# Optimization experiments

Hardware: AMD Instinct MI355X
Metric: run time of the kernel (lower is better)

The kernel has to match this reference:

```python
import jax, jax.numpy as jnp
import numpy as np

B, N, K, C = 4, 8192, 16, 64
HID, OUT = 128, 128


def setup_inputs() -> dict:
    key = jax.random.key(0)
    ks = jax.random.split(key, 8)
    f = jax.random.normal(ks[0], (B, N, C), dtype=jnp.float32)
    knn_idx = jax.random.randint(ks[1], (B, N, K), 0, N, dtype=jnp.int32)
    W1 = jax.random.normal(ks[2], (3 * C, HID), dtype=jnp.float32) * (1.0 / np.sqrt(3 * C))
    b1 = jnp.zeros((HID,), dtype=jnp.float32)
    W2 = jax.random.normal(ks[3], (HID, HID), dtype=jnp.float32) * (1.0 / np.sqrt(HID))
    b2 = jnp.zeros((HID,), dtype=jnp.float32)
    W3 = jax.random.normal(ks[4], (HID, OUT), dtype=jnp.float32) * 0.05  # init.normal_(std=0.05)
    b3 = jnp.zeros((OUT,), dtype=jnp.float32)  # init.zeros_
    return {"f": f, "knn_idx": knn_idx, "W1": W1, "b1": b1, "W2": W2, "b2": b2, "W3": W3, "b3": b3}


def reference(f, knn_idx, W1, b1, W2, b2, W3, b3):
    # knn_group: gather neighbor features -> [B, N, k, C]
    knn_feat = jax.vmap(lambda fb, ib: fb[ib])(f, knn_idx)
    f_tiled = jnp.broadcast_to(f[:, :, None, :], knn_feat.shape)  # [B,N,k,C]
    x = jnp.concatenate([f_tiled, knn_feat, knn_feat - f_tiled], axis=-1)  # [B,N,k,3C]
    x = jax.nn.relu(jnp.einsum('bnkc,ch->bnkh', x, W1) + b1)
    x = jax.nn.relu(jnp.einsum('bnkh,hg->bnkg', x, W2) + b2)
    x = jnp.max(x, axis=2)  # max-pool over k -> [B,N,HID]
    return jnp.einsum('bnh,ho->bno', x, W3) + b3
```

## Files before the change

### kernel.cpp

```cpp
#include <hip/hip_runtime.h>


#define BB 4
#define NN 8192
#define KK 16
#define CC 64
#define HH 128
#define ITERS 4

typedef _Float16 f16;
typedef __fp16 h16x2 __attribute__((ext_vector_type(2)));
typedef _Float16 f16x8 __attribute__((ext_vector_type(8)));
typedef float f32x4 __attribute__((ext_vector_type(4)));

#define MFMA16(a, b, c) __builtin_amdgcn_mfma_f32_16x16x32_f16(a, b, c, 0, 0, 0)

static __device__ __forceinline__ f16x8 cvt8(f32x4 a0, f32x4 a1) {
  h16x2 c0 = __builtin_amdgcn_cvt_pkrtz(a0[0], a0[1]);
  h16x2 c1 = __builtin_amdgcn_cvt_pkrtz(a0[2], a0[3]);
  h16x2 c2 = __builtin_amdgcn_cvt_pkrtz(a1[0], a1[1]);
  h16x2 c3 = __builtin_amdgcn_cvt_pkrtz(a1[2], a1[3]);
  f16x8 v;
  v[0] = (f16)c0[0]; v[1] = (f16)c0[1]; v[2] = (f16)c1[0]; v[3] = (f16)c1[1];
  v[4] = (f16)c2[0]; v[5] = (f16)c2[1]; v[6] = (f16)c3[0]; v[7] = (f16)c3[1];
  return v;
}

static __device__ __forceinline__ void lds_barrier() {
  asm volatile("s_waitcnt lgkmcnt(0)" ::: "memory");
  __builtin_amdgcn_s_barrier();
  __builtin_amdgcn_sched_barrier(0);
}

__global__ void prep_all(const float* __restrict__ f, const float* __restrict__ W1,
                         const float* __restrict__ W2, const float* __restrict__ W3,
                         f16* __restrict__ ws, f16* __restrict__ fh) {
  if (blockIdx.x < 12) {
    int fid = blockIdx.x * 8 + (threadIdx.x >> 6);
    int l = threadIdx.x & 63;
    int g = l >> 4, r = l & 15;
    f16x8 v;
#pragma unroll
    for (int j = 0; j < 8; ++j) {
      int kl = 16 * (j >> 2) + 4 * g + (j & 3);
      float x;
      if (fid < 16) {
        int ht = fid >> 1, kt = fid & 1, h = ht * 16 + r, k = kt * 32 + kl;
        x = W1[(64 + k) * HH + h] + W1[(128 + k) * HH + h];
      } else if (fid < 48) {
        int t = fid - 16, h2t = t >> 2, kt = t & 3;
        x = W2[(kt * 32 + kl) * HH + h2t * 16 + r];
      } else if (fid < 64) {
        int t = fid - 48, ht = t >> 1, kt = t & 1, h = ht * 16 + r, k = kt * 32 + kl;
        x = W1[k * HH + h] - W1[(128 + k) * HH + h];
      } else {
        int t = fid - 64, ot = t >> 2, kt = t & 3;
        x = W3[(kt * 32 + kl) * HH + ot * 16 + r];
      }
      v[j] = (f16)x;
    }
    *(f16x8*)(ws + (size_t)fid * 512 + l * 8) = v;
  } else {
    int chunk = (blockIdx.x - 12) * 512 + threadIdx.x;
    int row = chunk >> 3;
    int kt = (chunk >> 2) & 1;
    int g = chunk & 3;
    const float* src = f + (size_t)row * CC + kt * 32;
    f32x4 a0 = *(const f32x4*)(src + 4 * g);
    f32x4 a1 = *(const f32x4*)(src + 16 + 4 * g);
    f16x8 v;
#pragma unroll
    for (int j = 0; j < 4; ++j) { v[j] = (f16)a0[j]; v[4 + j] = (f16)a1[j]; }
    *(f16x8*)(fh + (size_t)row * CC + kt * 32 + g * 8) = v;
  }
}

__global__ __launch_bounds__(512, 4) void knn_pers(
    const int* __restrict__ knn, const float* __restrict__ b1,
    const float* __restrict__ b2, const float* __restrict__ b3,
    const f16* __restrict__ ws, const f16* __restrict__ fh,
    float* __restrict__ out) {
  extern __shared__ char smem[];
  f16* wbuf = (f16*)smem;
  float* fabuf = (float*)(wbuf + 48 * 512);
  f16* pooled = (f16*)(fabuf + 16 * 132);

  const int tid = threadIdx.x;
  const int wave = tid >> 6, lane = tid & 63;
  const int g = lane >> 4, r = lane & 15;

  const int wg = (blockIdx.x & 7) * 64 + (blockIdx.x >> 3);
  const int b = wg >> 7;
  const int nbase = (wg & 127) * 64;
  const f16* fhb = fh + (size_t)b * NN * CC;
  const int p0 = wave * 2;

  f16x8 st[6];
#pragma unroll
  for (int i = 0; i < 6; ++i)
    st[i] = *(const f16x8*)(ws + (size_t)(i * 512 + tid) * 8);
#pragma unroll
  for (int i = 0; i < 6; ++i)
    *(f16x8*)(wbuf + (size_t)(i * 512 + tid) * 8) = st[i];

  f16x8 aw[2], w3f[4];
#pragma unroll
  for (int kt = 0; kt < 2; ++kt)
    aw[kt] = *(const f16x8*)(ws + (size_t)(48 + wave * 2 + kt) * 512 + lane * 8);
#pragma unroll
  for (int kt = 0; kt < 4; ++kt)
    w3f[kt] = *(const f16x8*)(ws + (size_t)(64 + wave * 4 + kt) * 512 + lane * 8);

  int nidx[2];
#pragma unroll
  for (int pp = 0; pp < 2; ++pp)
    nidx[pp] = knn[(size_t)(b * NN + nbase + p0 + pp) * KK + r];
  f16x8 bfa[2];
  {
    const f16* fo16 = fhb + (size_t)(nbase + r) * CC;
    bfa[0] = *(const f16x8*)(fo16 + g * 8);
    bfa[1] = *(const f16x8*)(fo16 + 32 + g * 8);
  }
  f16x8 bf[2][2];
#pragma unroll
  for (int pp = 0; pp < 2; ++pp) {
    const f16* fn16 = fhb + (size_t)nidx[pp] * CC;
#pragma unroll
    for (int kt = 0; kt < 2; ++kt)
      bf[pp][kt] = *(const f16x8*)(fn16 + kt * 32 + g * 8);
  }

  for (int it = 0; it < ITERS; ++it) {
    const int n0 = nbase + it * 16;
    const int itn = (it < ITERS - 1) ? it + 1 : it;

    int nidxN[2];
#pragma unroll
    for (int pp = 0; pp < 2; ++pp)
      nidxN[pp] = knn[(size_t)(b * NN + nbase + itn * 16 + p0 + pp) * KK + r];

    {
      f32x4 acc = {0.f, 0.f, 0.f, 0.f};
      acc = MFMA16(aw[0], bfa[0], acc);
      acc = MFMA16(aw[1], bfa[1], acc);
      f32x4 b1v = *(const f32x4*)(b1 + wave * 16 + g * 4);
      f32x4 fa;
#pragma unroll
      for (int i = 0; i < 4; ++i) fa[i] = acc[i] + b1v[i];
      *(f32x4*)(fabuf + r * 132 + wave * 16 + g * 4) = fa;
    }

    lds_barrier();

    f16x8 h1f[2][4];
#pragma unroll
    for (int ht = 0; ht < 8; ++ht) {
      f32x4 acc[2] = {{0.f, 0.f, 0.f, 0.f}, {0.f, 0.f, 0.f, 0.f}};
#pragma unroll
      for (int kt = 0; kt < 2; ++kt) {
        f16x8 wfrag = *(const f16x8*)(wbuf + (size_t)(ht * 2 + kt) * 512 + lane * 8);
        acc[0] = MFMA16(wfrag, bf[0][kt], acc[0]);
        acc[1] = MFMA16(wfrag, bf[1][kt], acc[1]);
      }
      f32x4 fa0 = *(const f32x4*)(fabuf + (p0 + 0) * 132 + ht * 16 + g * 4);
      f32x4 fa1 = *(const f32x4*)(fabuf + (p0 + 1) * 132 + ht * 16 + g * 4);
#pragma unroll
      for (int pp = 0; pp < 2; ++pp) {
        const f32x4& fa = pp ? fa1 : fa0;
        float x0 = acc[pp][0] + fa[0]; x0 = x0 > 0.f ? x0 : 0.f;
        float x1 = acc[pp][1] + fa[1]; x1 = x1 > 0.f ? x1 : 0.f;
        float x2 = acc[pp][2] + fa[2]; x2 = x2 > 0.f ? x2 : 0.f;
        float x3 = acc[pp][3] + fa[3]; x3 = x3 > 0.f ? x3 : 0.f;
        h16x2 lo = __builtin_amdgcn_cvt_pkrtz(x0, x1);
        h16x2 hi = __builtin_amdgcn_cvt_pkrtz(x2, x3);
        h1f[pp][ht >> 1][(ht & 1) * 4 + 0] = (f16)lo[0];
        h1f[pp][ht >> 1][(ht & 1) * 4 + 1] = (f16)lo[1];
        h1f[pp][ht >> 1][(ht & 1) * 4 + 2] = (f16)hi[0];
        h1f[pp][ht >> 1][(ht & 1) * 4 + 3] = (f16)hi[1];
      }
    }

#pragma unroll
    for (int h2t = 0; h2t < 8; ++h2t) {
      f32x4 c0 = {0.f, 0.f, 0.f, 0.f}, c1 = {0.f, 0.f, 0.f, 0.f};
#pragma unroll
      for (int kt = 0; kt < 4; ++kt) {
        f16x8 w2f = *(const f16x8*)(wbuf + (size_t)(16 + h2t * 4 + kt) * 512 + lane * 8);
        c0 = MFMA16(h1f[0][kt], w2f, c0);
        c1 = MFMA16(h1f[1][kt], w2f, c1);
      }
      float b2v = b2[h2t * 16 + r];
#pragma unroll
      for (int pp = 0; pp < 2; ++pp) {
        f32x4 cc = pp ? c1 : c0;
        float m = fmaxf(fmaxf(cc[0], cc[1]), fmaxf(cc[2], cc[3]));
        m = fmaxf(m, __shfl_xor(m, 16, 64));
        m = fmaxf(m, __shfl_xor(m, 32, 64));
        float x = m + b2v;
        f16 pv = (f16)(x > 0.f ? x : 0.f);
        if (g == 0) {
          pooled[(h2t >> 1) * 512 + ((r >> 2) * 16 + p0 + pp) * 8 +
                 (h2t & 1) * 4 + (r & 3)] = pv;
        }
      }
    }

    f16x8 bfaN[2], bfN[2][2];
    {
      const f16* fo16 = fhb + (size_t)(nbase + itn * 16 + r) * CC;
      bfaN[0] = *(const f16x8*)(fo16 + g * 8);
      bfaN[1] = *(const f16x8*)(fo16 + 32 + g * 8);
    }
#pragma unroll
    for (int pp = 0; pp < 2; ++pp) {
      const f16* fn16 = fhb + (size_t)nidxN[pp] * CC;
#pragma unroll
      for (int kt = 0; kt < 2; ++kt)
        bfN[pp][kt] = *(const f16x8*)(fn16 + kt * 32 + g * 8);
    }

    lds_barrier();

    {
      f32x4 a3 = {0.f, 0.f, 0.f, 0.f};
#pragma unroll
      for (int kt = 0; kt < 4; ++kt) {
        f16x8 pf = *(const f16x8*)(pooled + kt * 512 + lane * 8);
        a3 = MFMA16(w3f[kt], pf, a3);
      }
      f32x4 b3v = *(const f32x4*)(b3 + wave * 16 + g * 4);
      f32x4 o;
#pragma unroll
      for (int i = 0; i < 4; ++i) o[i] = a3[i] + b3v[i];
      *(f32x4*)(out + ((size_t)b * NN + n0 + r) * HH + wave * 16 + g * 4) = o;
    }

    bfa[0] = bfaN[0]; bfa[1] = bfaN[1];
#pragma unroll
    for (int pp = 0; pp < 2; ++pp)
#pragma unroll
      for (int kt = 0; kt < 2; ++kt)
        bf[pp][kt] = bfN[pp][kt];
    nidx[0] = nidxN[0]; nidx[1] = nidxN[1];
  }
}

__global__ __launch_bounds__(512, 4) void knn_fb(
    const float* __restrict__ f, const int* __restrict__ knn,
    const float* __restrict__ b1, const float* __restrict__ b2,
    const float* __restrict__ b3, const f16* __restrict__ ws,
    float* __restrict__ out) {
  extern __shared__ char smem[];
  f16* wbuf = (f16*)smem;
  float* fabuf = (float*)(wbuf + 48 * 512);
  f16* pooled = (f16*)(fabuf + 16 * 132);

  const int tid = threadIdx.x;
  const int wave = tid >> 6, lane = tid & 63;
  const int g = lane >> 4, r = lane & 15;
  const int wg = (blockIdx.x & 7) * 256 + (blockIdx.x >> 3);
  const int b = wg >> 9;
  const int n0 = (wg & 511) * 16;
  const float* fb = f + (size_t)b * NN * CC;
  const int p0 = wave * 2;

  int nidx[2];
#pragma unroll
  for (int pp = 0; pp < 2; ++pp)
    nidx[pp] = knn[(size_t)(b * NN + n0 + p0 + pp) * KK + r];

  const float* fo = fb + (size_t)(n0 + r) * CC;
  f32x4 rawF[2][2];
#pragma unroll
  for (int kt = 0; kt < 2; ++kt) {
    rawF[kt][0] = *(const f32x4*)(fo + kt * 32 + 4 * g);
    rawF[kt][1] = *(const f32x4*)(fo + kt * 32 + 4 * g + 16);
  }
  f16x8 aw[2];
#pragma unroll
  for (int kt = 0; kt < 2; ++kt)
    aw[kt] = *(const f16x8*)(ws + (size_t)(48 + wave * 2 + kt) * 512 + lane * 8);

  f16x8 st[6];
#pragma unroll
  for (int i = 0; i < 6; ++i)
    st[i] = *(const f16x8*)(ws + (size_t)(i * 512 + tid) * 8);
#pragma unroll
  for (int i = 0; i < 6; ++i)
    *(f16x8*)(wbuf + (size_t)(i * 512 + tid) * 8) = st[i];

  f32x4 rawN[2][2][2];
#pragma unroll
  for (int pp = 0; pp < 2; ++pp) {
    const float* fn = fb + (size_t)nidx[pp] * CC;
#pragma unroll
    for (int kt = 0; kt < 2; ++kt) {
      rawN[pp][kt][0] = *(const f32x4*)(fn + kt * 32 + 4 * g);
      rawN[pp][kt][1] = *(const f32x4*)(fn + kt * 32 + 4 * g + 16);
    }
  }

  {
    f32x4 acc = {0.f, 0.f, 0.f, 0.f};
#pragma unroll
    for (int kt = 0; kt < 2; ++kt) {
      f16x8 bfa2 = cvt8(rawF[kt][0], rawF[kt][1]);
      acc = MFMA16(aw[kt], bfa2, acc);
    }
    f32x4 b1v = *(const f32x4*)(b1 + wave * 16 + g * 4);
    f32x4 fa;
#pragma unroll
    for (int i = 0; i < 4; ++i) fa[i] = acc[i] + b1v[i];
    *(f32x4*)(fabuf + r * 132 + wave * 16 + g * 4) = fa;
  }

  lds_barrier();

  f16x8 bf[2][2];
#pragma unroll
  for (int pp = 0; pp < 2; ++pp)
#pragma unroll
    for (int kt = 0; kt < 2; ++kt)
      bf[pp][kt] = cvt8(rawN[pp][kt][0], rawN[pp][kt][1]);

  f16x8 h1f[2][4];
#pragma unroll
  for (int ht = 0; ht < 8; ++ht) {
    f32x4 acc[2] = {{0.f, 0.f, 0.f, 0.f}, {0.f, 0.f, 0.f, 0.f}};
#pragma unroll
    for (int kt = 0; kt < 2; ++kt) {
      f16x8 wfrag = *(const f16x8*)(wbuf + (size_t)(ht * 2 + kt) * 512 + lane * 8);
      acc[0] = MFMA16(wfrag, bf[0][kt], acc[0]);
      acc[1] = MFMA16(wfrag, bf[1][kt], acc[1]);
    }
    f32x4 fa0 = *(const f32x4*)(fabuf + (p0 + 0) * 132 + ht * 16 + g * 4);
    f32x4 fa1 = *(const f32x4*)(fabuf + (p0 + 1) * 132 + ht * 16 + g * 4);
#pragma unroll
    for (int pp = 0; pp < 2; ++pp) {
      const f32x4& fa = pp ? fa1 : fa0;
      float x0 = acc[pp][0] + fa[0]; x0 = x0 > 0.f ? x0 : 0.f;
      float x1 = acc[pp][1] + fa[1]; x1 = x1 > 0.f ? x1 : 0.f;
      float x2 = acc[pp][2] + fa[2]; x2 = x2 > 0.f ? x2 : 0.f;
      float x3 = acc[pp][3] + fa[3]; x3 = x3 > 0.f ? x3 : 0.f;
      h16x2 lo = __builtin_amdgcn_cvt_pkrtz(x0, x1);
      h16x2 hi = __builtin_amdgcn_cvt_pkrtz(x2, x3);
      h1f[pp][ht >> 1][(ht & 1) * 4 + 0] = (f16)lo[0];
      h1f[pp][ht >> 1][(ht & 1) * 4 + 1] = (f16)lo[1];
      h1f[pp][ht >> 1][(ht & 1) * 4 + 2] = (f16)hi[0];
      h1f[pp][ht >> 1][(ht & 1) * 4 + 3] = (f16)hi[1];
    }
  }

#pragma unroll
  for (int h2t = 0; h2t < 8; ++h2t) {
    f32x4 c0 = {0.f, 0.f, 0.f, 0.f}, c1 = {0.f, 0.f, 0.f, 0.f};
#pragma unroll
    for (int kt = 0; kt < 4; ++kt) {
      f16x8 w2f = *(const f16x8*)(wbuf + (size_t)(16 + h2t * 4 + kt) * 512 + lane * 8);
      c0 = MFMA16(h1f[0][kt], w2f, c0);
      c1 = MFMA16(h1f[1][kt], w2f, c1);
    }
    float b2v = b2[h2t * 16 + r];
#pragma unroll
    for (int pp = 0; pp < 2; ++pp) {
      f32x4 cc = pp ? c1 : c0;
      float m = fmaxf(fmaxf(cc[0], cc[1]), fmaxf(cc[2], cc[3]));
      m = fmaxf(m, __shfl_xor(m, 16, 64));
      m = fmaxf(m, __shfl_xor(m, 32, 64));
      float x = m + b2v;
      f16 pv = (f16)(x > 0.f ? x : 0.f);
      if (g == 0) {
        pooled[(h2t >> 1) * 512 + ((r >> 2) * 16 + p0 + pp) * 8 +
               (h2t & 1) * 4 + (r & 3)] = pv;
      }
    }
  }

  f16x8 w3f[4];
#pragma unroll
  for (int kt = 0; kt < 4; ++kt)
    w3f[kt] = *(const f16x8*)(ws + (size_t)(64 + wave * 4 + kt) * 512 + lane * 8);

  lds_barrier();

  {
    f32x4 a3 = {0.f, 0.f, 0.f, 0.f};
#pragma unroll
    for (int kt = 0; kt < 4; ++kt) {
      f16x8 pf = *(const f16x8*)(pooled + kt * 512 + lane * 8);
      a3 = MFMA16(w3f[kt], pf, a3);
    }
    f32x4 b3v = *(const f32x4*)(b3 + wave * 16 + g * 4);
    f32x4 o;
#pragma unroll
    for (int i = 0; i < 4; ++i) o[i] = a3[i] + b3v[i];
    *(f32x4*)(out + ((size_t)b * NN + n0 + r) * HH + wave * 16 + g * 4) = o;
  }
}

extern "C" void kernel_launch(void* const* d_in, const int* in_sizes, int n_in,
                              void* d_out, int out_size, void* d_ws, size_t ws_size,
                              hipStream_t stream) {
  const float* f = (const float*)d_in[0];
  const int* knn = (const int*)d_in[1];
  const float* W1 = (const float*)d_in[2];
  const float* b1 = (const float*)d_in[3];
  const float* W2 = (const float*)d_in[4];
  const float* b2 = (const float*)d_in[5];
  const float* W3 = (const float*)d_in[6];
  const float* b3 = (const float*)d_in[7];
  float* outp = (float*)d_out;
  f16* wsp = (f16*)d_ws;
  f16* fh = wsp + 96 * 512;

  const size_t need = 96 * 1024 + (size_t)BB * NN * CC * 2;

  if (ws_size >= need) {
    (void)hipFuncSetAttribute((const void*)knn_pers,
                              hipFuncAttributeMaxDynamicSharedMemorySize, 61696);
    prep_all<<<12 + (BB * NN * 8) / 512, 512, 0, stream>>>(f, W1, W2, W3, wsp, fh);
    knn_pers<<<(BB * NN) / 64, 512, 61696, stream>>>(knn, b1, b2, b3, wsp, fh, outp);
  } else {
    (void)hipFuncSetAttribute((const void*)knn_fb,
                              hipFuncAttributeMaxDynamicSharedMemorySize, 61696);
    prep_all<<<12, 512, 0, stream>>>(f, W1, W2, W3, wsp, fh);
    knn_fb<<<(BB * NN) / 16, 512, 61696, stream>>>(f, knn, b1, b2, b3, wsp, outp);
  }
}
```

Baseline: 44.71 us.

## Double-buffer center-feature and pooled LDS buffers to drop one barrier per iteration

Result: slower. 47.61 us (+6.5%).

```diff
diff --git a/kernel.cpp b/kernel.cpp
--- a/kernel.cpp
+++ b/kernel.cpp
@@ -83,7 +83,7 @@
   extern __shared__ char smem[];
   f16* wbuf = (f16*)smem;
   float* fabuf = (float*)(wbuf + 48 * 512);
-  f16* pooled = (f16*)(fabuf + 16 * 132);
+  f16* pooled = (f16*)(fabuf + 2 * 16 * 132);
 
   const int tid = threadIdx.x;
   const int wave = tid >> 6, lane = tid & 63;
@@ -110,47 +110,57 @@
 #pragma unroll
   for (int kt = 0; kt < 4; ++kt)
     w3f[kt] = *(const f16x8*)(ws + (size_t)(64 + wave * 4 + kt) * 512 + lane * 8);
+  f32x4 b1v = *(const f32x4*)(b1 + wave * 16 + g * 4);
+  f32x4 b3v = *(const f32x4*)(b3 + wave * 16 + g * 4);
+  float b2v[8];
+#pragma unroll
+  for (int h2t = 0; h2t < 8; ++h2t) b2v[h2t] = b2[h2t * 16 + r];
 
   int nidx[2];
 #pragma unroll
   for (int pp = 0; pp < 2; ++pp)
     nidx[pp] = knn[(size_t)(b * NN + nbase + p0 + pp) * KK + r];
-  f16x8 bfa[2];
+  f16x8 bf[2][2];
+#pragma unroll
+  for (int pp = 0; pp < 2; ++pp) {
+    const f16* fn16 = fhb + (size_t)nidx[pp] * CC;
+#pragma unroll
+    for (int kt = 0; kt < 2; ++kt)
+      bf[pp][kt] = *(const f16x8*)(fn16 + kt * 32 + g * 8);
+  }
   {
     const f16* fo16 = fhb + (size_t)(nbase + r) * CC;
-    bfa[0] = *(const f16x8*)(fo16 + g * 8);
-    bfa[1] = *(const f16x8*)(fo16 + 32 + g * 8);
-  }
-  f16x8 bf[2][2];
-#pragma unroll
-  for (int pp = 0; pp < 2; ++pp) {
-    const f16* fn16 = fhb + (size_t)nidx[pp] * CC;
-#pragma unroll
-    for (int kt = 0; kt < 2; ++kt)
-      bf[pp][kt] = *(const f16x8*)(fn16 + kt * 32 + g * 8);
-  }
+    f16x8 a0 = *(const f16x8*)(fo16 + g * 8);
+    f16x8 a1 = *(const f16x8*)(fo16 + 32 + g * 8);
+    f32x4 acc = {0.f, 0.f, 0.f, 0.f};
+    acc = MFMA16(aw[0], a0, acc);
+    acc = MFMA16(aw[1], a1, acc);
+    f32x4 fa;
+#pragma unroll
+    for (int i = 0; i < 4; ++i) fa[i] = acc[i] + b1v[i];
+    *(f32x4*)(fabuf + r * 132 + wave * 16 + g * 4) = fa;
+  }
+
+  lds_barrier();
 
   for (int it = 0; it < ITERS; ++it) {
     const int n0 = nbase + it * 16;
     const int itn = (it < ITERS - 1) ? it + 1 : it;
+    const int cur = it & 1, nxt = (it + 1) & 1;
+    float* fabC = fabuf + cur * 2112;
+    float* fabN = fabuf + nxt * 2112;
+    f16* pooC = pooled + cur * 2048;
 
     int nidxN[2];
 #pragma unroll
     for (int pp = 0; pp < 2; ++pp)
       nidxN[pp] = knn[(size_t)(b * NN + nbase + itn * 16 + p0 + pp) * KK + r];
-
+    f16x8 bfaN0, bfaN1;
     {
-      f32x4 acc = {0.f, 0.f, 0.f, 0.f};
-      acc = MFMA16(aw[0], bfa[0], acc);
-      acc = MFMA16(aw[1], bfa[1], acc);
-      f32x4 b1v = *(const f32x4*)(b1 + wave * 16 + g * 4);
-      f32x4 fa;
-#pragma unroll
-      for (int i = 0; i < 4; ++i) fa[i] = acc[i] + b1v[i];
-      *(f32x4*)(fabuf + r * 132 + wave * 16 + g * 4) = fa;
-    }
-
-    lds_barrier();
+      const f16* fo16 = fhb + (size_t)(nbase + itn * 16 + r) * CC;
+      bfaN0 = *(const f16x8*)(fo16 + g * 8);
+      bfaN1 = *(const f16x8*)(fo16 + 32 + g * 8);
+    }
 
     f16x8 h1f[2][4];
 #pragma unroll
@@ -162,8 +172,8 @@
         acc[0] = MFMA16(wfrag, bf[0][kt], acc[0]);
         acc[1] = MFMA16(wfrag, bf[1][kt], acc[1]);
       }
-      f32x4 fa0 = *(const f32x4*)(fabuf + (p0 + 0) * 132 + ht * 16 + g * 4);
-      f32x4 fa1 = *(const f32x4*)(fabuf + (p0 + 1) * 132 + ht * 16 + g * 4);
+      f32x4 fa0 = *(const f32x4*)(fabC + (p0 + 0) * 132 + ht * 16 + g * 4);
+      f32x4 fa1 = *(const f32x4*)(fabC + (p0 + 1) * 132 + ht * 16 + g * 4);
 #pragma unroll
       for (int pp = 0; pp < 2; ++pp) {
         const f32x4& fa = pp ? fa1 : fa0;
@@ -189,28 +199,32 @@
         c0 = MFMA16(h1f[0][kt], w2f, c0);
         c1 = MFMA16(h1f[1][kt], w2f, c1);
       }
-      float b2v = b2[h2t * 16 + r];
 #pragma unroll
       for (int pp = 0; pp < 2; ++pp) {
         f32x4 cc = pp ? c1 : c0;
         float m = fmaxf(fmaxf(cc[0], cc[1]), fmaxf(cc[2], cc[3]));
         m = fmaxf(m, __shfl_xor(m, 16, 64));
         m = fmaxf(m, __shfl_xor(m, 32, 64));
-        float x = m + b2v;
+        float x = m + b2v[h2t];
         f16 pv = (f16)(x > 0.f ? x : 0.f);
         if (g == 0) {
-          pooled[(h2t >> 1) * 512 + ((r >> 2) * 16 + p0 + pp) * 8 +
-                 (h2t & 1) * 4 + (r & 3)] = pv;
+          pooC[(h2t >> 1) * 512 + ((r >> 2) * 16 + p0 + pp) * 8 +
+               (h2t & 1) * 4 + (r & 3)] = pv;
         }
       }
     }
 
-    f16x8 bfaN[2], bfN[2][2];
     {
-      const f16* fo16 = fhb + (size_t)(nbase + itn * 16 + r) * CC;
-      bfaN[0] = *(const f16x8*)(fo16 + g * 8);
-      bfaN[1] = *(const f16x8*)(fo16 + 32 + g * 8);
-    }
+      f32x4 acc = {0.f, 0.f, 0.f, 0.f};
+      acc = MFMA16(aw[0], bfaN0, acc);
+      acc = MFMA16(aw[1], bfaN1, acc);
+      f32x4 fa;
+#pragma unroll
+      for (int i = 0; i < 4; ++i) fa[i] = acc[i] + b1v[i];
+      *(f32x4*)(fabN + r * 132 + wave * 16 + g * 4) = fa;
+    }
+
+    f16x8 bfN[2][2];
 #pragma unroll
     for (int pp = 0; pp < 2; ++pp) {
       const f16* fn16 = fhb + (size_t)nidxN[pp] * CC;
@@ -225,17 +239,15 @@
       f32x4 a3 = {0.f, 0.f, 0.f, 0.f};
 #pragma unroll
       for (int kt = 0; kt < 4; ++kt) {
-        f16x8 pf = *(const f16x8*)(pooled + kt * 512 + lane * 8);
+        f16x8 pf = *(const f16x8*)(pooC + kt * 512 + lane * 8);
         a3 = MFMA16(w3f[kt], pf, a3);
       }
-      f32x4 b3v = *(const f32x4*)(b3 + wave * 16 + g * 4);
       f32x4 o;
 #pragma unroll
       for (int i = 0; i < 4; ++i) o[i] = a3[i] + b3v[i];
       *(f32x4*)(out + ((size_t)b * NN + n0 + r) * HH + wave * 16 + g * 4) = o;
     }
 
-    bfa[0] = bfaN[0]; bfa[1] = bfaN[1];
 #pragma unroll
     for (int pp = 0; pp < 2; ++pp)
 #pragma unroll
@@ -417,9 +429,9 @@
 
   if (ws_size >= need) {
     (void)hipFuncSetAttribute((const void*)knn_pers,
-                              hipFuncAttributeMaxDynamicSharedMemorySize, 61696);
+                              hipFuncAttributeMaxDynamicSharedMemorySize, 74240);
     prep_all<<<12 + (BB * NN * 8) / 512, 512, 0, stream>>>(f, W1, W2, W3, wsp, fh);
-    knn_pers<<<(BB * NN) / 64, 512, 61696, stream>>>(knn, b1, b2, b3, wsp, fh, outp);
+    knn_pers<<<(BB * NN) / 64, 512, 74240, stream>>>(knn, b1, b2, b3, wsp, fh, outp);
   } else {
     (void)hipFuncSetAttribute((const void*)knn_fb,
                               hipFuncAttributeMaxDynamicSharedMemorySize, 61696);
```

## Replace persistent 4-iteration loop with single-pass 32-point workgroups

Applied to the files above, without the earlier changes.

Result: slower. 50.92 us (+13.9%).

```diff
diff --git a/kernel.cpp b/kernel.cpp
--- a/kernel.cpp
+++ b/kernel.cpp
@@ -6,7 +6,6 @@
 #define KK 16
 #define CC 64
 #define HH 128
-#define ITERS 4
 
 typedef _Float16 f16;
 typedef __fp16 h16x2 __attribute__((ext_vector_type(2)));
@@ -75,7 +74,7 @@
   }
 }
 
-__global__ __launch_bounds__(512, 4) void knn_pers(
+__global__ __launch_bounds__(512, 4) void knn_main(
     const int* __restrict__ knn, const float* __restrict__ b1,
     const float* __restrict__ b2, const float* __restrict__ b3,
     const f16* __restrict__ ws, const f16* __restrict__ fh,
@@ -83,17 +82,22 @@
   extern __shared__ char smem[];
   f16* wbuf = (f16*)smem;
   float* fabuf = (float*)(wbuf + 48 * 512);
-  f16* pooled = (f16*)(fabuf + 16 * 132);
+  f16* pooled = (f16*)(fabuf + 32 * 132);
 
   const int tid = threadIdx.x;
   const int wave = tid >> 6, lane = tid & 63;
   const int g = lane >> 4, r = lane & 15;
 
-  const int wg = (blockIdx.x & 7) * 64 + (blockIdx.x >> 3);
-  const int b = wg >> 7;
-  const int nbase = (wg & 127) * 64;
+  const int wg = (blockIdx.x & 7) * 128 + (blockIdx.x >> 3);
+  const int b = wg >> 8;
+  const int n0 = (wg & 255) * 32;
   const f16* fhb = fh + (size_t)b * NN * CC;
-  const int p0 = wave * 2;
+  const int p0 = wave * 4;
+
+  int nidx[4];
+#pragma unroll
+  for (int pp = 0; pp < 4; ++pp)
+    nidx[pp] = knn[(size_t)(b * NN + n0 + p0 + pp) * KK + r];
 
   f16x8 st[6];
 #pragma unroll
@@ -103,145 +107,107 @@
   for (int i = 0; i < 6; ++i)
     *(f16x8*)(wbuf + (size_t)(i * 512 + tid) * 8) = st[i];
 
-  f16x8 aw[2], w3f[4];
-#pragma unroll
-  for (int kt = 0; kt < 2; ++kt)
-    aw[kt] = *(const f16x8*)(ws + (size_t)(48 + wave * 2 + kt) * 512 + lane * 8);
-#pragma unroll
-  for (int kt = 0; kt < 4; ++kt)
-    w3f[kt] = *(const f16x8*)(ws + (size_t)(64 + wave * 4 + kt) * 512 + lane * 8);
-
-  int nidx[2];
-#pragma unroll
-  for (int pp = 0; pp < 2; ++pp)
-    nidx[pp] = knn[(size_t)(b * NN + nbase + p0 + pp) * KK + r];
-  f16x8 bfa[2];
   {
-    const f16* fo16 = fhb + (size_t)(nbase + r) * CC;
-    bfa[0] = *(const f16x8*)(fo16 + g * 8);
-    bfa[1] = *(const f16x8*)(fo16 + 32 + g * 8);
-  }
-  f16x8 bf[2][2];
-#pragma unroll
-  for (int pp = 0; pp < 2; ++pp) {
+    f16x8 aw0 = *(const f16x8*)(ws + (size_t)(48 + wave * 2 + 0) * 512 + lane * 8);
+    f16x8 aw1 = *(const f16x8*)(ws + (size_t)(48 + wave * 2 + 1) * 512 + lane * 8);
+    f32x4 b1v = *(const f32x4*)(b1 + wave * 16 + g * 4);
+#pragma unroll
+    for (int gg = 0; gg < 2; ++gg) {
+      const f16* fo16 = fhb + (size_t)(n0 + gg * 16 + r) * CC;
+      f16x8 bo0 = *(const f16x8*)(fo16 + g * 8);
+      f16x8 bo1 = *(const f16x8*)(fo16 + 32 + g * 8);
+      f32x4 acc = {0.f, 0.f, 0.f, 0.f};
+      acc = MFMA16(aw0, bo0, acc);
+      acc = MFMA16(aw1, bo1, acc);
+      f32x4 fa;
+#pragma unroll
+      for (int i = 0; i < 4; ++i) fa[i] = acc[i] + b1v[i];
+      *(f32x4*)(fabuf + (gg * 16 + r) * 132 + wave * 16 + g * 4) = fa;
+    }
+  }
+
+  f16x8 bf[4][2];
+#pragma unroll
+  for (int pp = 0; pp < 4; ++pp) {
     const f16* fn16 = fhb + (size_t)nidx[pp] * CC;
-#pragma unroll
-    for (int kt = 0; kt < 2; ++kt)
-      bf[pp][kt] = *(const f16x8*)(fn16 + kt * 32 + g * 8);
-  }
-
-  for (int it = 0; it < ITERS; ++it) {
-    const int n0 = nbase + it * 16;
-    const int itn = (it < ITERS - 1) ? it + 1 : it;
-
-    int nidxN[2];
-#pragma unroll
-    for (int pp = 0; pp < 2; ++pp)
-      nidxN[pp] = knn[(size_t)(b * NN + nbase + itn * 16 + p0 + pp) * KK + r];
-
-    {
-      f32x4 acc = {0.f, 0.f, 0.f, 0.f};
-      acc = MFMA16(aw[0], bfa[0], acc);
-      acc = MFMA16(aw[1], bfa[1], acc);
-      f32x4 b1v = *(const f32x4*)(b1 + wave * 16 + g * 4);
-      f32x4 fa;
-#pragma unroll
-      for (int i = 0; i < 4; ++i) fa[i] = acc[i] + b1v[i];
-      *(f32x4*)(fabuf + r * 132 + wave * 16 + g * 4) = fa;
-    }
-
-    lds_barrier();
-
-    f16x8 h1f[2][4];
+    bf[pp][0] = *(const f16x8*)(fn16 + g * 8);
+    bf[pp][1] = *(const f16x8*)(fn16 + 32 + g * 8);
+  }
+
+  lds_barrier();
+
+  f16x8 h1f[4][4];
+#pragma unroll
+  for (int half = 0; half < 2; ++half) {
 #pragma unroll
     for (int ht = 0; ht < 8; ++ht) {
-      f32x4 acc[2] = {{0.f, 0.f, 0.f, 0.f}, {0.f, 0.f, 0.f, 0.f}};
+      f32x4 a0 = *(const f32x4*)(fabuf + (p0 + half * 2 + 0) * 132 + ht * 16 + g * 4);
+      f32x4 a1 = *(const f32x4*)(fabuf + (p0 + half * 2 + 1) * 132 + ht * 16 + g * 4);
 #pragma unroll
       for (int kt = 0; kt < 2; ++kt) {
         f16x8 wfrag = *(const f16x8*)(wbuf + (size_t)(ht * 2 + kt) * 512 + lane * 8);
-        acc[0] = MFMA16(wfrag, bf[0][kt], acc[0]);
-        acc[1] = MFMA16(wfrag, bf[1][kt], acc[1]);
-      }
-      f32x4 fa0 = *(const f32x4*)(fabuf + (p0 + 0) * 132 + ht * 16 + g * 4);
-      f32x4 fa1 = *(const f32x4*)(fabuf + (p0 + 1) * 132 + ht * 16 + g * 4);
-#pragma unroll
-      for (int pp = 0; pp < 2; ++pp) {
-        const f32x4& fa = pp ? fa1 : fa0;
-        float x0 = acc[pp][0] + fa[0]; x0 = x0 > 0.f ? x0 : 0.f;
-        float x1 = acc[pp][1] + fa[1]; x1 = x1 > 0.f ? x1 : 0.f;
-        float x2 = acc[pp][2] + fa[2]; x2 = x2 > 0.f ? x2 : 0.f;
-        float x3 = acc[pp][3] + fa[3]; x3 = x3 > 0.f ? x3 : 0.f;
+        a0 = MFMA16(wfrag, bf[half * 2 + 0][kt], a0);
+        a1 = MFMA16(wfrag, bf[half * 2 + 1][kt], a1);
+      }
+#pragma unroll
+      for (int q = 0; q < 2; ++q) {
+        f32x4 acc = q ? a1 : a0;
+        float x0 = acc[0] > 0.f ? acc[0] : 0.f;
+        float x1 = acc[1] > 0.f ? acc[1] : 0.f;
+        float x2 = acc[2] > 0.f ? acc[2] : 0.f;
+        float x3 = acc[3] > 0.f ? acc[3] : 0.f;
         h16x2 lo = __builtin_amdgcn_cvt_pkrtz(x0, x1);
         h16x2 hi = __builtin_amdgcn_cvt_pkrtz(x2, x3);
+        int pp = half * 2 + q;
         h1f[pp][ht >> 1][(ht & 1) * 4 + 0] = (f16)lo[0];
         h1f[pp][ht >> 1][(ht & 1) * 4 + 1] = (f16)lo[1];
         h1f[pp][ht >> 1][(ht & 1) * 4 + 2] = (f16)hi[0];
         h1f[pp][ht >> 1][(ht & 1) * 4 + 3] = (f16)hi[1];
       }
     }
-
-#pragma unroll
-    for (int h2t = 0; h2t < 8; ++h2t) {
-      f32x4 c0 = {0.f, 0.f, 0.f, 0.f}, c1 = {0.f, 0.f, 0.f, 0.f};
-#pragma unroll
-      for (int kt = 0; kt < 4; ++kt) {
-        f16x8 w2f = *(const f16x8*)(wbuf + (size_t)(16 + h2t * 4 + kt) * 512 + lane * 8);
-        c0 = MFMA16(h1f[0][kt], w2f, c0);
-        c1 = MFMA16(h1f[1][kt], w2f, c1);
-      }
-      float b2v = b2[h2t * 16 + r];
-#pragma unroll
-      for (int pp = 0; pp < 2; ++pp) {
-        f32x4 cc = pp ? c1 : c0;
-        float m = fmaxf(fmaxf(cc[0], cc[1]), fmaxf(cc[2], cc[3]));
-        m = fmaxf(m, __shfl_xor(m, 16, 64));
-        m = fmaxf(m, __shfl_xor(m, 32, 64));
-        float x = m + b2v;
-        f16 pv = (f16)(x > 0.f ? x : 0.f);
-        if (g == 0) {
-          pooled[(h2t >> 1) * 512 + ((r >> 2) * 16 + p0 + pp) * 8 +
-                 (h2t & 1) * 4 + (r & 3)] = pv;
-        }
-      }
-    }
-
-    f16x8 bfaN[2], bfN[2][2];
-    {
-      const f16* fo16 = fhb + (size_t)(nbase + itn * 16 + r) * CC;
-      bfaN[0] = *(const f16x8*)(fo16 + g * 8);
-      bfaN[1] = *(const f16x8*)(fo16 + 32 + g * 8);
-    }
-#pragma unroll
-    for (int pp = 0; pp < 2; ++pp) {
-      const f16* fn16 = fhb + (size_t)nidxN[pp] * CC;
-#pragma unroll
-      for (int kt = 0; kt < 2; ++kt)
-        bfN[pp][kt] = *(const f16x8*)(fn16 + kt * 32 + g * 8);
-    }
-
-    lds_barrier();
-
-    {
-      f32x4 a3 = {0.f, 0.f, 0.f, 0.f};
-#pragma unroll
-      for (int kt = 0; kt < 4; ++kt) {
-        f16x8 pf = *(const f16x8*)(pooled + kt * 512 + lane * 8);
-        a3 = MFMA16(w3f[kt], pf, a3);
-      }
-      f32x4 b3v = *(const f32x4*)(b3 + wave * 16 + g * 4);
-      f32x4 o;
-#pragma unroll
-      for (int i = 0; i < 4; ++i) o[i] = a3[i] + b3v[i];
-      *(f32x4*)(out + ((size_t)b * NN + n0 + r) * HH + wave * 16 + g * 4) = o;
-    }
-
-    bfa[0] = bfaN[0]; bfa[1] = bfaN[1];
-#pragma unroll
-    for (int pp = 0; pp < 2; ++pp)
-#pragma unroll
-      for (int kt = 0; kt < 2; ++kt)
-        bf[pp][kt] = bfN[pp][kt];
-    nidx[0] = nidxN[0]; nidx[1] = nidxN[1];
+  }
+
+  const int gg0 = wave >> 2;
+#pragma unroll
+  for (int h2t = 0; h2t < 8; ++h2t) {
+    f32x4 c[4];
+#pragma unroll
+    for (int pp = 0; pp < 4; ++pp) c[pp] = (f32x4){0.f, 0.f, 0.f, 0.f};
+#pragma unroll
+    for (int kt = 0; kt < 4; ++kt) {
+      f16x8 w2f = *(const f16x8*)(wbuf + (size_t)(16 + h2t * 4 + kt) * 512 + lane * 8);
+#pragma unroll
+      for (int pp = 0; pp < 4; ++pp) c[pp] = MFMA16(h1f[pp][kt], w2f, c[pp]);
+    }
+    float b2v = b2[h2t * 16 + r];
+#pragma unroll
+    for (int pp = 0; pp < 4; ++pp) {
+      float m = fmaxf(fmaxf(c[pp][0], c[pp][1]), fmaxf(c[pp][2], c[pp][3]));
+      m = fmaxf(m, __shfl_xor(m, 16, 64));
+      m = fmaxf(m, __shfl_xor(m, 32, 64));
+      float x = m + b2v;
+      f16 pv = (f16)(x > 0.f ? x : 0.f);
+      if (g == 0) {
+        int p = (p0 + pp) & 15;
+        pooled[gg0 * 2048 + (h2t >> 1) * 512 + ((r >> 2) * 16 + p) * 8 +
+               (h2t & 1) * 4 + (r & 3)] = pv;
+      }
+    }
+  }
+
+  lds_barrier();
+
+  f32x4 b3v = *(const f32x4*)(b3 + wave * 16 + g * 4);
+#pragma unroll
+  for (int gg = 0; gg < 2; ++gg) {
+    f32x4 a3 = b3v;
+#pragma unroll
+    for (int kt = 0; kt < 4; ++kt) {
+      f16x8 w3f = *(const f16x8*)(ws + (size_t)(64 + wave * 4 + kt) * 512 + lane * 8);
+      f16x8 pf = *(const f16x8*)(pooled + gg * 2048 + kt * 512 + lane * 8);
+      a3 = MFMA16(w3f, pf, a3);
+    }
+    *(f32x4*)(out + ((size_t)b * NN + n0 + gg * 16 + r) * HH + wave * 16 + g * 4) = a3;
   }
 }
 
@@ -416,10 +382,10 @@
   const size_t need = 96 * 1024 + (size_t)BB * NN * CC * 2;
 
   if (ws_size >= need) {
-    (void)hipFuncSetAttribute((const void*)knn_pers,
-                              hipFuncAttributeMaxDynamicSharedMemorySize, 61696);
+    (void)hipFuncSetAttribute((const void*)knn_main,
+                              hipFuncAttributeMaxDynamicSharedMemorySize, 74240);
     prep_all<<<12 + (BB * NN * 8) / 512, 512, 0, stream>>>(f, W1, W2, W3, wsp, fh);
-    knn_pers<<<(BB * NN) / 64, 512, 61696, stream>>>(knn, b1, b2, b3, wsp, fh, outp);
+    knn_main<<<(BB * NN) / 32, 512, 74240, stream>>>(knn, b1, b2, b3, wsp, fh, outp);
   } else {
     (void)hipFuncSetAttribute((const void*)knn_fb,
                               hipFuncAttributeMaxDynamicSharedMemorySize, 61696);
```
